# Performance work log

Hardware: AMD Instinct MI355X
Metric: run time of the kernel (lower is better)

## Reference

```python
import jax, jax.numpy as jnp
import numpy as np

K = 15
LAM = 1.0
EPS = 1e-8


def _pdist(a):
    # pairwise euclidean distance (torch.cdist p=2), safe sqrt (zero grad at 0)
    sq = jnp.sum(a * a, axis=1)
    d2 = sq[:, None] + sq[None, :] - 2.0 * (a @ a.T)
    d2 = jnp.maximum(d2, 0.0)
    pos = d2 > 0
    return jnp.where(pos, jnp.sqrt(jnp.where(pos, d2, 1.0)), 0.0)


def _knn_distance_loss(z, xf, k):
    B = xf.shape[0]
    x_dist = _pdist(xf)
    z_dist = _pdist(z)
    eye = jnp.eye(B, dtype=bool)
    x_noself = jnp.where(eye, jnp.inf, x_dist)
    # k smallest per row -> top_k of negated distances
    _, knn_idx = jax.lax.top_k(-x_noself, k)          # (B, k)
    rows = jnp.arange(B)[:, None]
    mask = jnp.zeros((B, B), dtype=bool).at[rows, knn_idx].set(True)
    mask = mask | mask.T                              # symmetric kNN mask
    x_m = jnp.where(mask, x_dist, 0.0)
    z_m = jnp.where(mask, z_dist, 0.0)
    x_norm = x_m / (jnp.max(x_m) + EPS)
    z_norm = z_m / (jnp.max(z_m) + EPS)
    diff2 = jnp.where(mask, (z_norm - x_norm) ** 2, 0.0)
    return diff2.sum() / mask.sum().astype(diff2.dtype)


def _forward(x, We1, be1, We2, be2, Wd1, bd1, Wd2, bd2):
    h = jax.nn.relu(x @ We1 + be1)
    z = h @ We2 + be2                                  # (B, latent)
    h2 = jax.nn.relu(z @ Wd1 + bd1)
    x_rec = h2 @ Wd2 + bd2
    rec_loss = jnp.mean((x_rec - x) ** 2)
    dist_loss = _knn_distance_loss(z, x.reshape(x.shape[0], -1), K)
    return rec_loss + LAM * dist_loss


def setup_inputs() -> dict:
    key = jax.random.key(0)
    ks = jax.random.split(key, 5)
    B, D, H, L = 8192, 1024, 512, 64
    s = 0.02
    return {
        "x": jax.random.normal(ks[0], (B, D), dtype=jnp.float32),
        "We1": jax.random.normal(ks[1], (D, H), dtype=jnp.float32) * s,
        "be1": jnp.zeros((H,), dtype=jnp.float32),
        "We2": jax.random.normal(ks[2], (H, L), dtype=jnp.float32) * s,
        "be2": jnp.zeros((L,), dtype=jnp.float32),
        "Wd1": jax.random.normal(ks[3], (L, H), dtype=jnp.float32) * s,
        "bd1": jnp.zeros((H,), dtype=jnp.float32),
        "Wd2": jax.random.normal(ks[4], (H, D), dtype=jnp.float32) * s,
        "bd2": jnp.zeros((D,), dtype=jnp.float32),
    }


def reference(x, We1, be1, We2, be2, Wd1, bd1, Wd2, bd2):
    return _forward(x, We1, be1, We2, be2, Wd1, bd1, Wd2, bd2)
```

## Files before the change

kernel.cpp:

```cpp
#include <hip/hip_runtime.h>

#define BB 8192
#define DD 1024
#define HH 512
#define LL 64
#define KNN 15
#define NT 64
#define NTILES 2080
#define NG1 256
#define NEDGE (BB * KNN)

typedef __attribute__((ext_vector_type(4))) float f32x4;
typedef __attribute__((ext_vector_type(8))) short s16x8;
typedef __attribute__((ext_vector_type(8))) unsigned short u16x8;
typedef __attribute__((ext_vector_type(4))) unsigned short u16x4;
typedef __attribute__((ext_vector_type(4))) _Float16 f16x4;

typedef s16x8 fragT;

__device__ __forceinline__ unsigned short f2bf(float f) {
  unsigned u = __float_as_uint(f);
  return (unsigned short)((u + 0x7fffu + ((u >> 16) & 1u)) >> 16);
}

__device__ __forceinline__ void gload16(const void* g, void* l) {
  __builtin_amdgcn_global_load_lds((const __attribute__((address_space(1))) unsigned int*)g,
                                   (__attribute__((address_space(3))) unsigned int*)l, 16, 0, 0);
}

__device__ __forceinline__ float unpack_d2(unsigned u) {
  _Float16 h = __builtin_bit_cast(_Float16, (unsigned short)(u >> 16));
  return (float)h;
}

__device__ __forceinline__ void ins15(unsigned (&l)[KNN], unsigned u) {
  if (u < l[KNN - 1]) {
    unsigned v = u;
#pragma unroll
    for (int p = 0; p < KNN; ++p) {
      unsigned lo = min(v, l[p]);
      unsigned hi = max(v, l[p]);
      l[p] = lo;
      v = hi;
    }
  }
}

__global__ void k_convert(const float* __restrict__ x, unsigned short* __restrict__ xb,
                          float* __restrict__ sqx) {
  int row = blockIdx.x;
  int t = threadIdx.x;
  f32x4 v = *(const f32x4*)(x + (size_t)row * DD + t * 4);
  u16x4 o;
  float s = 0.f;
#pragma unroll
  for (int j = 0; j < 4; ++j) {
    float f = v[j];
    s += f * f;
    o[j] = f2bf(f);
  }
  *(u16x4*)(xb + (size_t)row * DD + t * 4) = o;
#pragma unroll
  for (int off = 32; off >= 1; off >>= 1) s += __shfl_down(s, off);
  __shared__ float ps[4];
  if ((t & 63) == 0) ps[t >> 6] = s;
  __syncthreads();
  if (t == 0) sqx[row] = ps[0] + ps[1] + ps[2] + ps[3];
}

__global__ void k_wt(const float* __restrict__ W, unsigned short* __restrict__ Wt, int Kd, int N) {
  __shared__ unsigned short T[64][65];
  int k0 = blockIdx.x * 64, n0 = blockIdx.y * 64;
  int t = threadIdx.x;
  int kr = t >> 4, nc = (t & 15) * 4;
#pragma unroll
  for (int q = 0; q < 4; ++q) {
    int k = kr + q * 16;
    f32x4 v = *(const f32x4*)(W + (size_t)(k0 + k) * N + n0 + nc);
#pragma unroll
    for (int j = 0; j < 4; ++j) T[nc + j][k] = f2bf(v[j]);
  }
  __syncthreads();
#pragma unroll
  for (int q = 0; q < 2; ++q) {
    int s = t + q * 256;
    int n = s >> 3, c = (s & 7) * 8;
    u16x8 o;
#pragma unroll
    for (int j = 0; j < 8; ++j) o[j] = T[n][c + j];
    *(u16x8*)(Wt + (size_t)(n0 + n) * Kd + k0 + c) = o;
  }
}

template <int NF, int RELU, int FUSE, int STF32, int STBF>
__device__ __forceinline__ void mgemm_body(
    char* LB, int m0, int n0,
    const unsigned short* __restrict__ A, const unsigned short* __restrict__ Wt,
    const float* __restrict__ bias, unsigned short* __restrict__ Cb, float* __restrict__ Cf,
    const float* __restrict__ Xref, float* __restrict__ rec_sum, int N, int Kd) {
  unsigned short* At = (unsigned short*)LB;
  unsigned short* Bt = (unsigned short*)(LB + 16384);
  int t = threadIdx.x;
  int lane = t & 63, w = t >> 6;
  int wr = w >> 1, wc = w & 1;
  int wbase = w * 64;

  int srow[4], ksh[4];
#pragma unroll
  for (int q = 0; q < 4; ++q) {
    int s = q * 256 + t;
    int r = s >> 3, g = s & 7;
    srow[q] = r;
    ksh[q] = (g ^ (r & 7)) * 8;
  }

  int lrow = lane & 15;
  int klo = (lane >> 4) << 4;
  int sw = (lane & 7) << 4;

  f32x4 acc[4][NF] = {};

  int ksteps = Kd >> 6;
  for (int kt = 0; kt < ksteps; ++kt) {
    int kb = kt << 6;
#pragma unroll
    for (int q = 0; q < 4; ++q)
      gload16(A + (size_t)(m0 + srow[q]) * Kd + kb + ksh[q], At + (q * 256 + wbase) * 8);
#pragma unroll
    for (int q = 0; q < NF; ++q)
      gload16(Wt + (size_t)(n0 + srow[q]) * Kd + kb + ksh[q], Bt + (q * 256 + wbase) * 8);
    __syncthreads();
#pragma unroll
    for (int kh = 0; kh < 2; ++kh) {
      int kbyte = ((kh << 6) | klo) ^ sw;
      fragT af[4], bf[NF];
#pragma unroll
      for (int m = 0; m < 4; ++m)
        af[m] = *(const fragT*)((const char*)At + (wr * 64 + m * 16 + lrow) * 128 + kbyte);
#pragma unroll
      for (int n = 0; n < NF; ++n)
        bf[n] = *(const fragT*)((const char*)Bt + (wc * NF * 16 + n * 16 + lrow) * 128 + kbyte);
#pragma unroll
      for (int m = 0; m < 4; ++m)
#pragma unroll
        for (int n = 0; n < NF; ++n)
          acc[m][n] = __builtin_amdgcn_mfma_f32_16x16x32_bf16(af[m], bf[n], acc[m][n], 0, 0, 0);
    }
    __syncthreads();
  }

  float local = 0.f;
#pragma unroll
  for (int m = 0; m < 4; ++m) {
    int row0 = m0 + wr * 64 + m * 16 + ((lane >> 4) << 2);
#pragma unroll
    for (int n = 0; n < NF; ++n) {
      int col = n0 + wc * NF * 16 + n * 16 + lrow;
      float bv = bias[col];
      f32x4 a = acc[m][n];
#pragma unroll
      for (int j = 0; j < 4; ++j) {
        float c = a[j] + bv;
        if (RELU) c = fmaxf(c, 0.f);
        if (FUSE) {
          float xv = Xref[(size_t)(row0 + j) * N + col];
          float d = c - xv;
          local = fmaf(d, d, local);
        }
        if (STBF) Cb[(size_t)(row0 + j) * N + col] = f2bf(c);
        if (STF32) Cf[(size_t)(row0 + j) * N + col] = c;
      }
    }
  }
  if (FUSE) {
#pragma unroll
    for (int off = 32; off >= 1; off >>= 1) local += __shfl_down(local, off);
    __shared__ float rs[4];
    if ((t & 63) == 0) rs[t >> 6] = local;
    __syncthreads();
    if (t == 0) atomicAdd(rec_sum, rs[0] + rs[1] + rs[2] + rs[3]);
  }
}

template <int NF, int RELU, int FUSE, int STF32, int STBF>
__global__ __launch_bounds__(256) void k_mgemm(
    const unsigned short* __restrict__ A, const unsigned short* __restrict__ Wt,
    const float* __restrict__ bias, unsigned short* __restrict__ Cb, float* __restrict__ Cf,
    const float* __restrict__ Xref, float* __restrict__ rec_sum, int N, int Kd) {
  __shared__ __attribute__((aligned(16))) char LB[16384 + NF * 32 * 128];
  mgemm_body<NF, RELU, FUSE, STF32, STBF>(LB, blockIdx.y * 128, blockIdx.x * (NF * 32),
                                          A, Wt, bias, Cb, Cf, Xref, rec_sum, N, Kd);
}

__global__ __launch_bounds__(256, 3) void k_gram_topk(
    const unsigned short* __restrict__ xb, const float* __restrict__ sqx,
    unsigned* __restrict__ part,
    const unsigned short* __restrict__ Wt1, const float* __restrict__ be1,
    unsigned short* __restrict__ hb) {
  __shared__ __attribute__((aligned(16))) char LB[33792];

  int bid0 = blockIdx.x;
  if (bid0 < NG1) {
    mgemm_body<4, 1, 0, 0, 1>(LB, (bid0 >> 2) * 128, (bid0 & 3) * 128,
                              xb, Wt1, be1, hb, nullptr, nullptr, nullptr, HH, DD);
    return;
  }

  unsigned short* At = (unsigned short*)LB;
  unsigned short* Bt = (unsigned short*)(LB + 16384);
  char* Sf = LB;
  unsigned* scratch = (unsigned*)(LB + 16384);
  float* sqr = (float*)(LB + 32768);
  float* sqc = (float*)(LB + 33280);

  int g = bid0 - NG1;
  int k = g & 7, m = g >> 3;
  int nA = 6 + 4 * (61 - 4 * k);
  int b, mm;
  if (m < nA) { b = k; mm = m; }
  else        { b = 15 - k; mm = m - nA; }
  int ctl, j;
  if (mm < 6) {
    if (mm < 1)      { ctl = 0; j = mm; }
    else if (mm < 3) { ctl = 1; j = mm - 1; }
    else             { ctl = 2; j = mm - 3; }
  } else {
    ctl = 3 + ((mm - 6) >> 2);
    j = (mm - 6) & 3;
  }
  int rt = 4 * b + j;
  int ct = 4 * b + ctl;
  bool diag = (rt == ct);
  int r0 = rt * 128, c0 = ct * 128;

  int t = threadIdx.x;
  int lane = t & 63, w = t >> 6;
  int wr = w >> 1, wc = w & 1;
  int wbase = w * 64;

  if (t < 128) {
    sqr[t] = sqx[r0 + t];
    sqc[t] = sqx[c0 + t];
  }

  int srow[4], ksh[4];
#pragma unroll
  for (int q = 0; q < 4; ++q) {
    int s = q * 256 + t;
    int r = s >> 3, gg = s & 7;
    srow[q] = r;
    ksh[q] = (gg ^ (r & 7)) * 8;
  }

  int lrow = lane & 15;
  int klo = (lane >> 4) << 4;
  int sw = (lane & 7) << 4;

  f32x4 acc[16] = {};

  for (int kt = 0; kt < 16; ++kt) {
    int kb = kt << 6;
#pragma unroll
    for (int q = 0; q < 4; ++q) {
      gload16(xb + (size_t)(r0 + srow[q]) * DD + kb + ksh[q], At + (q * 256 + wbase) * 8);
      gload16(xb + (size_t)(c0 + srow[q]) * DD + kb + ksh[q], Bt + (q * 256 + wbase) * 8);
    }
    __syncthreads();
#pragma unroll
    for (int kh = 0; kh < 2; ++kh) {
      int kbyte = ((kh << 6) | klo) ^ sw;
      fragT af[4], bf[4];
#pragma unroll
      for (int mq = 0; mq < 4; ++mq)
        af[mq] = *(const fragT*)((const char*)At + (wr * 64 + mq * 16 + lrow) * 128 + kbyte);
#pragma unroll
      for (int n = 0; n < 4; ++n)
        bf[n] = *(const fragT*)((const char*)Bt + (wc * 64 + n * 16 + lrow) * 128 + kbyte);
#pragma unroll
      for (int mq = 0; mq < 4; ++mq)
#pragma unroll
        for (int n = 0; n < 4; ++n)
          acc[mq * 4 + n] =
              __builtin_amdgcn_mfma_f32_16x16x32_bf16(af[mq], bf[n], acc[mq * 4 + n], 0, 0, 0);
    }
    __syncthreads();
  }

  unsigned rowlist[KNN];
#pragma unroll
  for (int p = 0; p < KNN; ++p) rowlist[p] = 0xFFFFFFFFu;

  int scanrow = t & 127, side = t >> 7;

#pragma unroll
  for (int nh = 0; nh < 2; ++nh) {
    if (wc == nh) {
#pragma unroll
      for (int mq = 0; mq < 4; ++mq) {
        int row0 = wr * 64 + mq * 16 + ((lane >> 4) << 2);
        f32x4 sq4 = *(const f32x4*)&sqr[row0];
#pragma unroll
        for (int n = 0; n < 4; ++n) {
          int colL = n * 16 + lrow;
          float sc = sqc[nh * 64 + colL];
          f32x4 a = acc[mq * 4 + n];
          f16x4 hv;
#pragma unroll
          for (int r = 0; r < 4; ++r) {
            float d2 = fmaxf(sq4[r] + sc - 2.f * a[r], 0.f);
            if (diag && (row0 + r == nh * 64 + colL)) d2 = 60000.f;
            hv[r] = (_Float16)d2;
          }
          *(f16x4*)(Sf + colL * 256 + (((row0 * 2)) ^ ((colL & 31) << 3))) = hv;
        }
      }
    }
    __syncthreads();
    {
      int cbase = side * 32;
      int jbase = c0 + nh * 64;
      for (int cc = 0; cc < 32; ++cc) {
        int colL = cbase + cc;
        unsigned bits = *(const unsigned short*)(Sf + colL * 256 +
                                                 ((scanrow * 2) ^ ((colL & 31) << 3)));
        ins15(rowlist, (bits << 16) | (unsigned)(jbase + colL));
      }
    }
    if (!diag) {
      int c = t & 63, seg = t >> 6;
      unsigned collist[KNN];
#pragma unroll
      for (int p = 0; p < KNN; ++p) collist[p] = 0xFFFFFFFFu;
      for (int rq = 0; rq < 8; ++rq) {
        int r = seg * 32 + rq * 4;
        u16x4 v4 = *(const u16x4*)(Sf + c * 256 + ((r * 2) ^ ((c & 31) << 3)));
#pragma unroll
        for (int jj = 0; jj < 4; ++jj)
          ins15(collist, ((unsigned)v4[jj] << 16) | (unsigned)(r0 + r + jj));
      }
      __syncthreads();
#pragma unroll
      for (int p = 0; p < KNN; ++p) scratch[(c * 4 + seg) * KNN + p] = collist[p];
      __syncthreads();
      if (t < 64) {
        unsigned fin[KNN];
#pragma unroll
        for (int p = 0; p < KNN; ++p) fin[p] = 0xFFFFFFFFu;
        for (int s = 0; s < 4; ++s)
#pragma unroll
          for (int p = 0; p < KNN; ++p) ins15(fin, scratch[(t * 4 + s) * KNN + p]);
        int jj = c0 + nh * 64 + t;
#pragma unroll
        for (int p = 0; p < KNN; ++p) part[((size_t)(rt * KNN + p)) * BB + jj] = fin[p];
      }
    }
    __syncthreads();
  }

#pragma unroll
  for (int p = 0; p < KNN; ++p) scratch[(scanrow * 2 + side) * KNN + p] = rowlist[p];
  __syncthreads();
  if (t < 128) {
    unsigned fin[KNN];
#pragma unroll
    for (int p = 0; p < KNN; ++p) fin[p] = 0xFFFFFFFFu;
    for (int s = 0; s < 2; ++s)
#pragma unroll
      for (int p = 0; p < KNN; ++p) ins15(fin, scratch[(t * 2 + s) * KNN + p]);
    int i = r0 + t;
#pragma unroll
    for (int p = 0; p < KNN; ++p) part[((size_t)(ct * KNN + p)) * BB + i] = fin[p];
  }
}

__global__ void k_merge1(const unsigned* __restrict__ part, unsigned* __restrict__ part2) {
  int gid = blockIdx.x * 256 + threadIdx.x;
  int s = gid >> 13, i = gid & 8191;
  unsigned l[KNN];
#pragma unroll
  for (int p = 0; p < KNN; ++p) l[p] = 0xFFFFFFFFu;
  for (int b = s * 16; b < s * 16 + 16; ++b)
    for (int p = 0; p < KNN; ++p) ins15(l, part[((size_t)(b * KNN + p)) * BB + i]);
#pragma unroll
  for (int p = 0; p < KNN; ++p) part2[((size_t)(s * KNN + p)) * BB + i] = l[p];
}

__global__ void k_merge2(const unsigned* __restrict__ part2, float* __restrict__ knn_d2,
                         int* __restrict__ knn_idx, unsigned* __restrict__ Mdir,
                         int* __restrict__ xmax_bits) {
  int i = blockIdx.x * 256 + threadIdx.x;
  unsigned l[KNN];
#pragma unroll
  for (int p = 0; p < KNN; ++p) l[p] = 0xFFFFFFFFu;
  for (int q = 0; q < 4 * KNN; ++q) ins15(l, part2[(size_t)q * BB + i]);
  float mx = 0.f;
#pragma unroll
  for (int p = 0; p < KNN; ++p) {
    unsigned u = l[p];
    float d = fmaxf(unpack_d2(u), 0.f);
    int j = (int)(u & 0xFFFFu);
    mx = fmaxf(mx, d);
    knn_d2[(size_t)i * KNN + p] = d;
    knn_idx[(size_t)i * KNN + p] = j;
    atomicOr(&Mdir[(size_t)i * (BB / 32) + (j >> 5)], 1u << (j & 31));
  }
  int t = threadIdx.x;
#pragma unroll
  for (int off = 32; off >= 1; off >>= 1) mx = fmaxf(mx, __shfl_down(mx, off));
  __shared__ float rm[4];
  if ((t & 63) == 0) rm[t >> 6] = mx;
  __syncthreads();
  if (t == 0) {
    float mb = fmaxf(fmaxf(rm[0], rm[1]), fmaxf(rm[2], rm[3]));
    atomicMax(xmax_bits, __float_as_int(mb));
  }
}

__global__ void k_edge_z(const float* __restrict__ z, const int* __restrict__ knn_idx,
                         float* __restrict__ zd2) {
  int e = blockIdx.x * 16 + (threadIdx.x >> 4);
  int sl = threadIdx.x & 15;
  int i = e / KNN;
  int j = knn_idx[e];
  f32x4 zi = *(const f32x4*)(z + (size_t)i * LL + sl * 4);
  f32x4 zj = *(const f32x4*)(z + (size_t)j * LL + sl * 4);
  float v = 0.f;
#pragma unroll
  for (int d = 0; d < 4; ++d) {
    float df = zi[d] - zj[d];
    v = fmaf(df, df, v);
  }
  v += __shfl_down(v, 8);
  v += __shfl_down(v, 4);
  v += __shfl_down(v, 2);
  v += __shfl_down(v, 1);
  if (sl == 0) zd2[e] = v;
}

__global__ void k_zmax(const float* __restrict__ zd2, int* __restrict__ zmax_bits) {
  int t = threadIdx.x;
  int idx = blockIdx.x * 256 + t;
  float mx = 0.f;
  for (int e = idx; e < NEDGE; e += 120 * 256) mx = fmaxf(mx, zd2[e]);
#pragma unroll
  for (int off = 32; off >= 1; off >>= 1) mx = fmaxf(mx, __shfl_down(mx, off));
  __shared__ float rm[4];
  if ((t & 63) == 0) rm[t >> 6] = mx;
  __syncthreads();
  if (t == 0) {
    float m = fmaxf(fmaxf(rm[0], rm[1]), fmaxf(rm[2], rm[3]));
    atomicMax(zmax_bits, __float_as_int(m));
  }
}

__global__ void k_loss(const float* __restrict__ knn_d2, const int* __restrict__ knn_idx,
                       const float* __restrict__ zd2, const unsigned* __restrict__ Mdir,
                       const int* __restrict__ xmax_bits, const int* __restrict__ zmax_bits,
                       float* __restrict__ loss_sum, float* __restrict__ cnt_sum) {
  int e = blockIdx.x * 256 + threadIdx.x;
  float inv_x = 1.f / (sqrtf(__int_as_float(*xmax_bits)) + 1e-8f);
  float inv_z = 1.f / (sqrtf(__int_as_float(*zmax_bits)) + 1e-8f);
  int i = e / KNN;
  int j = knn_idx[e];
  unsigned bit = (Mdir[(size_t)j * (BB / 32) + (i >> 5)] >> (i & 31)) & 1u;
  float wgt = bit ? 1.f : 2.f;
  float xd = sqrtf(knn_d2[e]);
  float zd = sqrtf(fmaxf(zd2[e], 0.f));
  float diff = zd * inv_z - xd * inv_x;
  float c1 = wgt * diff * diff;
  float c2 = wgt;
#pragma unroll
  for (int off = 32; off >= 1; off >>= 1) {
    c1 += __shfl_down(c1, off);
    c2 += __shfl_down(c2, off);
  }
  __shared__ float r1[4], r2[4];
  int t = threadIdx.x;
  if ((t & 63) == 0) { r1[t >> 6] = c1; r2[t >> 6] = c2; }
  __syncthreads();
  if (t == 0) {
    atomicAdd(loss_sum, r1[0] + r1[1] + r1[2] + r1[3]);
    atomicAdd(cnt_sum, r2[0] + r2[1] + r2[2] + r2[3]);
  }
}

__global__ void k_final(const float* __restrict__ rec_sum, const float* __restrict__ loss_sum,
                        const float* __restrict__ cnt_sum, float* __restrict__ out) {
  if (threadIdx.x == 0)
    out[0] = rec_sum[0] * (1.f / 8388608.f) + loss_sum[0] / cnt_sum[0];
}

extern "C" void kernel_launch(void* const* d_in, const int* in_sizes, int n_in,
                              void* d_out, int out_size, void* d_ws, size_t ws_size,
                              hipStream_t stream) {
  const float* x = (const float*)d_in[0];
  const float* We1 = (const float*)d_in[1];
  const float* be1 = (const float*)d_in[2];
  const float* We2 = (const float*)d_in[3];
  const float* be2 = (const float*)d_in[4];
  const float* Wd1 = (const float*)d_in[5];
  const float* bd1 = (const float*)d_in[6];
  const float* Wd2 = (const float*)d_in[7];
  const float* bd2 = (const float*)d_in[8];

  char* ws = (char*)d_ws;
  size_t off = 0;
  auto alloc = [&](size_t bytes) {
    void* p = ws + off;
    off += (bytes + 255) & ~(size_t)255;
    return p;
  };
  unsigned short* xb = (unsigned short*)alloc((size_t)BB * DD * 2);
  unsigned short* hb = (unsigned short*)alloc((size_t)BB * HH * 2);
  unsigned short* zb = (unsigned short*)alloc((size_t)BB * LL * 2);
  unsigned short* h2b = (unsigned short*)alloc((size_t)BB * HH * 2);
  float* z = (float*)alloc((size_t)BB * LL * 4);
  float* sqx = (float*)alloc((size_t)BB * 4);
  unsigned short* Wt1 = (unsigned short*)alloc((size_t)HH * DD * 2);
  unsigned short* Wt2 = (unsigned short*)alloc((size_t)LL * HH * 2);
  unsigned short* Wt3 = (unsigned short*)alloc((size_t)HH * LL * 2);
  unsigned short* Wt4 = (unsigned short*)alloc((size_t)DD * HH * 2);
  unsigned* part = (unsigned*)alloc((size_t)NT * KNN * BB * 4);
  unsigned* part2 = (unsigned*)alloc((size_t)4 * KNN * BB * 4);
  float* knn_d2 = (float*)alloc((size_t)BB * KNN * 4);
  int* knn_idx = (int*)alloc((size_t)BB * KNN * 4);
  float* zd2 = (float*)alloc((size_t)BB * KNN * 4);
  unsigned* Mdir = (unsigned*)alloc((size_t)BB * (BB / 32) * 4);
  float* scal = (float*)alloc(64);
  float* rec_sum = scal + 0;
  float* loss_sum = scal + 1;
  float* cnt_sum = scal + 2;
  int* xmax_bits = (int*)(scal + 3);
  int* zmax_bits = (int*)(scal + 4);

  hipMemsetAsync(Mdir, 0, (size_t)BB * (BB / 32) * 4, stream);
  hipMemsetAsync(scal, 0, 64, stream);

  k_convert<<<BB, 256, 0, stream>>>(x, xb, sqx);
  k_wt<<<dim3(DD / 64, HH / 64), 256, 0, stream>>>(We1, Wt1, DD, HH);
  k_wt<<<dim3(HH / 64, LL / 64), 256, 0, stream>>>(We2, Wt2, HH, LL);
  k_wt<<<dim3(LL / 64, HH / 64), 256, 0, stream>>>(Wd1, Wt3, LL, HH);
  k_wt<<<dim3(HH / 64, DD / 64), 256, 0, stream>>>(Wd2, Wt4, HH, DD);

  k_gram_topk<<<NG1 + NTILES, 256, 0, stream>>>(xb, sqx, part, Wt1, be1, hb);

  k_mgemm<2, 0, 0, 1, 1><<<dim3(LL / 64, BB / 128), 256, 0, stream>>>(
      hb, Wt2, be2, zb, z, nullptr, nullptr, LL, HH);
  k_mgemm<4, 1, 0, 0, 1><<<dim3(HH / 128, BB / 128), 256, 0, stream>>>(
      zb, Wt3, bd1, h2b, nullptr, nullptr, nullptr, HH, LL);
  k_mgemm<4, 0, 1, 0, 0><<<dim3(DD / 128, BB / 128), 256, 0, stream>>>(
      h2b, Wt4, bd2, nullptr, nullptr, x, rec_sum, DD, HH);

  k_merge1<<<128, 256, 0, stream>>>(part, part2);
  k_merge2<<<BB / 256, 256, 0, stream>>>(part2, knn_d2, knn_idx, Mdir, xmax_bits);
  k_edge_z<<<NEDGE / 16, 256, 0, stream>>>(z, knn_idx, zd2);
  k_zmax<<<120, 256, 0, stream>>>(zd2, zmax_bits);
  k_loss<<<NEDGE / 256, 256, 0, stream>>>(knn_d2, knn_idx, zd2, Mdir, xmax_bits, zmax_bits,
                                          loss_sum, cnt_sum);
  k_final<<<1, 64, 0, stream>>>(rec_sum, loss_sum, cnt_sum, (float*)d_out);
}
```

Measured before the change: 390.2 us.

## Fuse prep kernels, early-exit top-k merges, and replace bitmask loss with algebraic edge sums

Merges the x conversion and four weight transposes into one launch. Adds batch-of-4 minimum prefilters in the top-k scans and early-break merging of the sorted partial lists. Drops the 8 MB dense kNN bitmask, its memset and its atomics, and detects reciprocal edges by checking neighbour j's list with a wave ballot. Expands the normalized squared difference into zz, xx and xz sums so edge distance, z max and loss collapse into one pass plus a final reduce. In exchange, expanding the square can cancel catastrophically in float32, and the extra gathers of knn_idx add memory traffic.

```diff
diff --git a/kernel.cpp b/kernel.cpp
--- a/kernel.cpp
+++ b/kernel.cpp
@@ -9,6 +9,7 @@
 #define NTILES 2080
 #define NG1 256
 #define NEDGE (BB * KNN)
+#define NEBLK (NEDGE / 128)
 
 typedef __attribute__((ext_vector_type(4))) float f32x4;
 typedef __attribute__((ext_vector_type(8))) short s16x8;
@@ -46,32 +47,44 @@
   }
 }
 
-__global__ void k_convert(const float* __restrict__ x, unsigned short* __restrict__ xb,
-                          float* __restrict__ sqx) {
-  int row = blockIdx.x;
+__global__ void k_prep(const float* __restrict__ x, unsigned short* __restrict__ xb,
+                       float* __restrict__ sqx,
+                       const float* __restrict__ We1, const float* __restrict__ We2,
+                       const float* __restrict__ Wd1, const float* __restrict__ Wd2,
+                       unsigned short* __restrict__ Wt1, unsigned short* __restrict__ Wt2,
+                       unsigned short* __restrict__ Wt3, unsigned short* __restrict__ Wt4) {
+  __shared__ float ps[4];
+  __shared__ unsigned short T[64][65];
+  int b = blockIdx.x;
   int t = threadIdx.x;
-  f32x4 v = *(const f32x4*)(x + (size_t)row * DD + t * 4);
-  u16x4 o;
-  float s = 0.f;
-#pragma unroll
-  for (int j = 0; j < 4; ++j) {
-    float f = v[j];
-    s += f * f;
-    o[j] = f2bf(f);
-  }
-  *(u16x4*)(xb + (size_t)row * DD + t * 4) = o;
-#pragma unroll
-  for (int off = 32; off >= 1; off >>= 1) s += __shfl_down(s, off);
-  __shared__ float ps[4];
-  if ((t & 63) == 0) ps[t >> 6] = s;
-  __syncthreads();
-  if (t == 0) sqx[row] = ps[0] + ps[1] + ps[2] + ps[3];
-}
-
-__global__ void k_wt(const float* __restrict__ W, unsigned short* __restrict__ Wt, int Kd, int N) {
-  __shared__ unsigned short T[64][65];
-  int k0 = blockIdx.x * 64, n0 = blockIdx.y * 64;
-  int t = threadIdx.x;
+  if (b < BB) {
+    f32x4 v = *(const f32x4*)(x + (size_t)b * DD + t * 4);
+    u16x4 o;
+    float s = 0.f;
+#pragma unroll
+    for (int j = 0; j < 4; ++j) {
+      float f = v[j];
+      s += f * f;
+      o[j] = f2bf(f);
+    }
+    *(u16x4*)(xb + (size_t)b * DD + t * 4) = o;
+#pragma unroll
+    for (int off = 32; off >= 1; off >>= 1) s += __shfl_down(s, off);
+    if ((t & 63) == 0) ps[t >> 6] = s;
+    __syncthreads();
+    if (t == 0) sqx[b] = ps[0] + ps[1] + ps[2] + ps[3];
+    return;
+  }
+  int c = b - BB;
+  const float* W;
+  unsigned short* Wt;
+  int Kd, N, idx;
+  if (c < 128)      { W = We1; Wt = Wt1; Kd = DD; N = HH; idx = c; }
+  else if (c < 136) { W = We2; Wt = Wt2; Kd = HH; N = LL; idx = c - 128; }
+  else if (c < 144) { W = Wd1; Wt = Wt3; Kd = LL; N = HH; idx = c - 136; }
+  else              { W = Wd2; Wt = Wt4; Kd = HH; N = DD; idx = c - 144; }
+  int nx = Kd >> 6;
+  int k0 = (idx % nx) * 64, n0 = (idx / nx) * 64;
   int kr = t >> 4, nc = (t & 15) * 4;
 #pragma unroll
   for (int q = 0; q < 4; ++q) {
@@ -84,11 +97,11 @@
 #pragma unroll
   for (int q = 0; q < 2; ++q) {
     int s = t + q * 256;
-    int n = s >> 3, c = (s & 7) * 8;
+    int n = s >> 3, cc = (s & 7) * 8;
     u16x8 o;
 #pragma unroll
-    for (int j = 0; j < 8; ++j) o[j] = T[n][c + j];
-    *(u16x8*)(Wt + (size_t)(n0 + n) * Kd + k0 + c) = o;
+    for (int j = 0; j < 8; ++j) o[j] = T[n][cc + j];
+    *(u16x8*)(Wt + (size_t)(n0 + n) * Kd + k0 + cc) = o;
   }
 }
 
@@ -319,11 +332,20 @@
     {
       int cbase = side * 32;
       int jbase = c0 + nh * 64;
-      for (int cc = 0; cc < 32; ++cc) {
-        int colL = cbase + cc;
-        unsigned bits = *(const unsigned short*)(Sf + colL * 256 +
-                                                 ((scanrow * 2) ^ ((colL & 31) << 3)));
-        ins15(rowlist, (bits << 16) | (unsigned)(jbase + colL));
+      for (int cc = 0; cc < 32; cc += 4) {
+        unsigned u[4];
+#pragma unroll
+        for (int q = 0; q < 4; ++q) {
+          int colL = cbase + cc + q;
+          unsigned bits = *(const unsigned short*)(Sf + colL * 256 +
+                                                   ((scanrow * 2) ^ ((colL & 31) << 3)));
+          u[q] = (bits << 16) | (unsigned)(jbase + colL);
+        }
+        unsigned m4 = min(min(u[0], u[1]), min(u[2], u[3]));
+        if (m4 < rowlist[KNN - 1]) {
+#pragma unroll
+          for (int q = 0; q < 4; ++q) ins15(rowlist, u[q]);
+        }
       }
     }
     if (!diag) {
@@ -334,9 +356,14 @@
       for (int rq = 0; rq < 8; ++rq) {
         int r = seg * 32 + rq * 4;
         u16x4 v4 = *(const u16x4*)(Sf + c * 256 + ((r * 2) ^ ((c & 31) << 3)));
-#pragma unroll
-        for (int jj = 0; jj < 4; ++jj)
-          ins15(collist, ((unsigned)v4[jj] << 16) | (unsigned)(r0 + r + jj));
+        unsigned u[4];
+#pragma unroll
+        for (int jj = 0; jj < 4; ++jj) u[jj] = ((unsigned)v4[jj] << 16) | (unsigned)(r0 + r + jj);
+        unsigned m4 = min(min(u[0], u[1]), min(u[2], u[3]));
+        if (m4 < collist[KNN - 1]) {
+#pragma unroll
+          for (int jj = 0; jj < 4; ++jj) ins15(collist, u[jj]);
+        }
       }
       __syncthreads();
 #pragma unroll
@@ -379,30 +406,48 @@
   unsigned l[KNN];
 #pragma unroll
   for (int p = 0; p < KNN; ++p) l[p] = 0xFFFFFFFFu;
-  for (int b = s * 16; b < s * 16 + 16; ++b)
-    for (int p = 0; p < KNN; ++p) ins15(l, part[((size_t)(b * KNN + p)) * BB + i]);
+  for (int b = s * 16; b < s * 16 + 16; ++b) {
+    size_t base = (size_t)(b * KNN) * BB + i;
+    unsigned u = part[base];
+    if (u < l[KNN - 1]) {
+      ins15(l, u);
+      for (int p = 1; p < KNN; ++p) {
+        u = part[base + (size_t)p * BB];
+        if (u >= l[KNN - 1]) break;
+        ins15(l, u);
+      }
+    }
+  }
 #pragma unroll
   for (int p = 0; p < KNN; ++p) part2[((size_t)(s * KNN + p)) * BB + i] = l[p];
 }
 
 __global__ void k_merge2(const unsigned* __restrict__ part2, float* __restrict__ knn_d2,
-                         int* __restrict__ knn_idx, unsigned* __restrict__ Mdir,
-                         int* __restrict__ xmax_bits) {
+                         int* __restrict__ knn_idx, int* __restrict__ xmax_bits) {
   int i = blockIdx.x * 256 + threadIdx.x;
   unsigned l[KNN];
 #pragma unroll
   for (int p = 0; p < KNN; ++p) l[p] = 0xFFFFFFFFu;
-  for (int q = 0; q < 4 * KNN; ++q) ins15(l, part2[(size_t)q * BB + i]);
+  for (int q = 0; q < 4; ++q) {
+    size_t base = (size_t)(q * KNN) * BB + i;
+    unsigned u = part2[base];
+    if (u < l[KNN - 1]) {
+      ins15(l, u);
+      for (int p = 1; p < KNN; ++p) {
+        u = part2[base + (size_t)p * BB];
+        if (u >= l[KNN - 1]) break;
+        ins15(l, u);
+      }
+    }
+  }
   float mx = 0.f;
 #pragma unroll
   for (int p = 0; p < KNN; ++p) {
     unsigned u = l[p];
     float d = fmaxf(unpack_d2(u), 0.f);
-    int j = (int)(u & 0xFFFFu);
     mx = fmaxf(mx, d);
     knn_d2[(size_t)i * KNN + p] = d;
-    knn_idx[(size_t)i * KNN + p] = j;
-    atomicOr(&Mdir[(size_t)i * (BB / 32) + (j >> 5)], 1u << (j & 31));
+    knn_idx[(size_t)i * KNN + p] = (int)(u & 0xFFFFu);
   }
   int t = threadIdx.x;
 #pragma unroll
@@ -416,78 +461,106 @@
   }
 }
 
-__global__ void k_edge_z(const float* __restrict__ z, const int* __restrict__ knn_idx,
-                         float* __restrict__ zd2) {
-  int e = blockIdx.x * 16 + (threadIdx.x >> 4);
-  int sl = threadIdx.x & 15;
-  int i = e / KNN;
-  int j = knn_idx[e];
-  f32x4 zi = *(const f32x4*)(z + (size_t)i * LL + sl * 4);
-  f32x4 zj = *(const f32x4*)(z + (size_t)j * LL + sl * 4);
-  float v = 0.f;
-#pragma unroll
-  for (int d = 0; d < 4; ++d) {
-    float df = zi[d] - zj[d];
-    v = fmaf(df, df, v);
-  }
-  v += __shfl_down(v, 8);
-  v += __shfl_down(v, 4);
-  v += __shfl_down(v, 2);
-  v += __shfl_down(v, 1);
-  if (sl == 0) zd2[e] = v;
-}
-
-__global__ void k_zmax(const float* __restrict__ zd2, int* __restrict__ zmax_bits) {
+__global__ void k_edge(const float* __restrict__ z, const int* __restrict__ knn_idx,
+                       const float* __restrict__ knn_d2, float* __restrict__ pzz,
+                       float* __restrict__ pxx, float* __restrict__ pxz,
+                       float* __restrict__ pcnt, float* __restrict__ pzm) {
   int t = threadIdx.x;
-  int idx = blockIdx.x * 256 + t;
-  float mx = 0.f;
-  for (int e = idx; e < NEDGE; e += 120 * 256) mx = fmaxf(mx, zd2[e]);
-#pragma unroll
-  for (int off = 32; off >= 1; off >>= 1) mx = fmaxf(mx, __shfl_down(mx, off));
-  __shared__ float rm[4];
-  if ((t & 63) == 0) rm[t >> 6] = mx;
+  int g = t >> 4, L = t & 15;
+  int lane = t & 63;
+  float szz = 0.f, sxx = 0.f, sxz = 0.f, scnt = 0.f, zm = 0.f;
+#pragma unroll
+  for (int pass = 0; pass < 8; ++pass) {
+    int e = blockIdx.x * 128 + pass * 16 + g;
+    int i = e / KNN;
+    int j = knn_idx[e];
+    f32x4 zi = *(const f32x4*)(z + (size_t)i * LL + L * 4);
+    f32x4 zj = *(const f32x4*)(z + (size_t)j * LL + L * 4);
+    float v = 0.f;
+#pragma unroll
+    for (int d = 0; d < 4; ++d) {
+      float df = zi[d] - zj[d];
+      v = fmaf(df, df, v);
+    }
+    v += __shfl_down(v, 8);
+    v += __shfl_down(v, 4);
+    v += __shfl_down(v, 2);
+    v += __shfl_down(v, 1);
+    int cand = (L < KNN) ? knn_idx[(size_t)j * KNN + L] : -1;
+    unsigned long long ball = __ballot(cand == i);
+    unsigned recip = (unsigned)(ball >> (lane & 48)) & 0xFFFFu;
+    if (L == 0) {
+      float w = recip ? 1.f : 2.f;
+      float xd2 = knn_d2[e];
+      szz = fmaf(w, v, szz);
+      sxx = fmaf(w, xd2, sxx);
+      sxz = fmaf(w, sqrtf(v * xd2), sxz);
+      scnt += w;
+      zm = fmaxf(zm, v);
+    }
+  }
+#pragma unroll
+  for (int off = 32; off >= 1; off >>= 1) {
+    szz += __shfl_down(szz, off);
+    sxx += __shfl_down(sxx, off);
+    sxz += __shfl_down(sxz, off);
+    scnt += __shfl_down(scnt, off);
+    zm = fmaxf(zm, __shfl_down(zm, off));
+  }
+  __shared__ float r[5][4];
+  int w4 = t >> 6;
+  if (lane == 0) {
+    r[0][w4] = szz; r[1][w4] = sxx; r[2][w4] = sxz; r[3][w4] = scnt; r[4][w4] = zm;
+  }
   __syncthreads();
   if (t == 0) {
-    float m = fmaxf(fmaxf(rm[0], rm[1]), fmaxf(rm[2], rm[3]));
-    atomicMax(zmax_bits, __float_as_int(m));
-  }
-}
-
-__global__ void k_loss(const float* __restrict__ knn_d2, const int* __restrict__ knn_idx,
-                       const float* __restrict__ zd2, const unsigned* __restrict__ Mdir,
-                       const int* __restrict__ xmax_bits, const int* __restrict__ zmax_bits,
-                       float* __restrict__ loss_sum, float* __restrict__ cnt_sum) {
-  int e = blockIdx.x * 256 + threadIdx.x;
-  float inv_x = 1.f / (sqrtf(__int_as_float(*xmax_bits)) + 1e-8f);
-  float inv_z = 1.f / (sqrtf(__int_as_float(*zmax_bits)) + 1e-8f);
-  int i = e / KNN;
-  int j = knn_idx[e];
-  unsigned bit = (Mdir[(size_t)j * (BB / 32) + (i >> 5)] >> (i & 31)) & 1u;
-  float wgt = bit ? 1.f : 2.f;
-  float xd = sqrtf(knn_d2[e]);
-  float zd = sqrtf(fmaxf(zd2[e], 0.f));
-  float diff = zd * inv_z - xd * inv_x;
-  float c1 = wgt * diff * diff;
-  float c2 = wgt;
+    pzz[blockIdx.x] = r[0][0] + r[0][1] + r[0][2] + r[0][3];
+    pxx[blockIdx.x] = r[1][0] + r[1][1] + r[1][2] + r[1][3];
+    pxz[blockIdx.x] = r[2][0] + r[2][1] + r[2][2] + r[2][3];
+    pcnt[blockIdx.x] = r[3][0] + r[3][1] + r[3][2] + r[3][3];
+    pzm[blockIdx.x] = fmaxf(fmaxf(r[4][0], r[4][1]), fmaxf(r[4][2], r[4][3]));
+  }
+}
+
+__global__ void k_final(const float* __restrict__ pzz, const float* __restrict__ pxx,
+                        const float* __restrict__ pxz, const float* __restrict__ pcnt,
+                        const float* __restrict__ pzm, const int* __restrict__ xmax_bits,
+                        const float* __restrict__ rec_sum, float* __restrict__ out) {
+  int t = threadIdx.x;
+  float szz = 0.f, sxx = 0.f, sxz = 0.f, scnt = 0.f, zm = 0.f;
+  for (int bb = t; bb < NEBLK; bb += 256) {
+    szz += pzz[bb];
+    sxx += pxx[bb];
+    sxz += pxz[bb];
+    scnt += pcnt[bb];
+    zm = fmaxf(zm, pzm[bb]);
+  }
 #pragma unroll
   for (int off = 32; off >= 1; off >>= 1) {
-    c1 += __shfl_down(c1, off);
-    c2 += __shfl_down(c2, off);
-  }
-  __shared__ float r1[4], r2[4];
-  int t = threadIdx.x;
-  if ((t & 63) == 0) { r1[t >> 6] = c1; r2[t >> 6] = c2; }
+    szz += __shfl_down(szz, off);
+    sxx += __shfl_down(sxx, off);
+    sxz += __shfl_down(sxz, off);
+    scnt += __shfl_down(scnt, off);
+    zm = fmaxf(zm, __shfl_down(zm, off));
+  }
+  __shared__ float r[5][4];
+  int w4 = t >> 6;
+  if ((t & 63) == 0) {
+    r[0][w4] = szz; r[1][w4] = sxx; r[2][w4] = sxz; r[3][w4] = scnt; r[4][w4] = zm;
+  }
   __syncthreads();
   if (t == 0) {
-    atomicAdd(loss_sum, r1[0] + r1[1] + r1[2] + r1[3]);
-    atomicAdd(cnt_sum, r2[0] + r2[1] + r2[2] + r2[3]);
-  }
-}
-
-__global__ void k_final(const float* __restrict__ rec_sum, const float* __restrict__ loss_sum,
-                        const float* __restrict__ cnt_sum, float* __restrict__ out) {
-  if (threadIdx.x == 0)
-    out[0] = rec_sum[0] * (1.f / 8388608.f) + loss_sum[0] / cnt_sum[0];
+    float SZZ = r[0][0] + r[0][1] + r[0][2] + r[0][3];
+    float SXX = r[1][0] + r[1][1] + r[1][2] + r[1][3];
+    float SXZ = r[2][0] + r[2][1] + r[2][2] + r[2][3];
+    float CNT = r[3][0] + r[3][1] + r[3][2] + r[3][3];
+    float ZM = fmaxf(fmaxf(r[4][0], r[4][1]), fmaxf(r[4][2], r[4][3]));
+    float xmax = __int_as_float(*xmax_bits);
+    float a = 1.f / (sqrtf(ZM) + 1e-8f);
+    float bq = 1.f / (sqrtf(xmax) + 1e-8f);
+    float loss = (a * a * SZZ + bq * bq * SXX - 2.f * a * bq * SXZ) / CNT;
+    out[0] = rec_sum[0] * (1.f / 8388608.f) + loss;
+  }
 }
 
 extern "C" void kernel_launch(void* const* d_in, const int* in_sizes, int n_in,
@@ -524,23 +597,18 @@
   unsigned* part2 = (unsigned*)alloc((size_t)4 * KNN * BB * 4);
   float* knn_d2 = (float*)alloc((size_t)BB * KNN * 4);
   int* knn_idx = (int*)alloc((size_t)BB * KNN * 4);
-  float* zd2 = (float*)alloc((size_t)BB * KNN * 4);
-  unsigned* Mdir = (unsigned*)alloc((size_t)BB * (BB / 32) * 4);
+  float* pzz = (float*)alloc(NEBLK * 4);
+  float* pxx = (float*)alloc(NEBLK * 4);
+  float* pxz = (float*)alloc(NEBLK * 4);
+  float* pcnt = (float*)alloc(NEBLK * 4);
+  float* pzm = (float*)alloc(NEBLK * 4);
   float* scal = (float*)alloc(64);
   float* rec_sum = scal + 0;
-  float* loss_sum = scal + 1;
-  float* cnt_sum = scal + 2;
-  int* xmax_bits = (int*)(scal + 3);
-  int* zmax_bits = (int*)(scal + 4);
-
-  hipMemsetAsync(Mdir, 0, (size_t)BB * (BB / 32) * 4, stream);
+  int* xmax_bits = (int*)(scal + 1);
+
   hipMemsetAsync(scal, 0, 64, stream);
 
-  k_convert<<<BB, 256, 0, stream>>>(x, xb, sqx);
-  k_wt<<<dim3(DD / 64, HH / 64), 256, 0, stream>>>(We1, Wt1, DD, HH);
-  k_wt<<<dim3(HH / 64, LL / 64), 256, 0, stream>>>(We2, Wt2, HH, LL);
-  k_wt<<<dim3(LL / 64, HH / 64), 256, 0, stream>>>(Wd1, Wt3, LL, HH);
-  k_wt<<<dim3(HH / 64, DD / 64), 256, 0, stream>>>(Wd2, Wt4, HH, DD);
+  k_prep<<<BB + 272, 256, 0, stream>>>(x, xb, sqx, We1, We2, Wd1, Wd2, Wt1, Wt2, Wt3, Wt4);
 
   k_gram_topk<<<NG1 + NTILES, 256, 0, stream>>>(xb, sqx, part, Wt1, be1, hb);
 
@@ -552,10 +620,7 @@
       h2b, Wt4, bd2, nullptr, nullptr, x, rec_sum, DD, HH);
 
   k_merge1<<<128, 256, 0, stream>>>(part, part2);
-  k_merge2<<<BB / 256, 256, 0, stream>>>(part2, knn_d2, knn_idx, Mdir, xmax_bits);
-  k_edge_z<<<NEDGE / 16, 256, 0, stream>>>(z, knn_idx, zd2);
-  k_zmax<<<120, 256, 0, stream>>>(zd2, zmax_bits);
-  k_loss<<<NEDGE / 256, 256, 0, stream>>>(knn_d2, knn_idx, zd2, Mdir, xmax_bits, zmax_bits,
-                                          loss_sum, cnt_sum);
-  k_final<<<1, 64, 0, stream>>>(rec_sum, loss_sum, cnt_sum, (float*)d_out);
-}
+  k_merge2<<<BB / 256, 256, 0, stream>>>(part2, knn_d2, knn_idx, xmax_bits);
+  k_edge<<<NEBLK, 256, 0, stream>>>(z, knn_idx, knn_d2, pzz, pxx, pxz, pcnt, pzm);
+  k_final<<<1, 256, 0, stream>>>(pzz, pxx, pxz, pcnt, pzm, xmax_bits, rec_sum, (float*)d_out);
+}
```

New measurement: 325.6 us. 1.2x faster.
